# Performance work log

Hardware: AMD Instinct MI355X
Metric: run time of the kernel (lower is better)

Reference implementation:

```python
import jax, jax.numpy as jnp
import numpy as np

INPUT_DIM = 1024
OUTPUT_DIM = 1024
DEGREE = 8


def setup_inputs() -> dict:
    key = jax.random.key(0)
    k1, k2 = jax.random.split(key)
    x = jax.random.normal(k1, (8192, INPUT_DIM), dtype=jnp.float32)
    std = 1.0 / (INPUT_DIM * (DEGREE + 1))
    cheby_coeffs = jax.random.normal(k2, (INPUT_DIM, OUTPUT_DIM, DEGREE + 1), dtype=jnp.float32) * std
    return {"x": x, "cheby_coeffs": cheby_coeffs}


def reference(x, cheby_coeffs):
    # x: [B, I]; cheby_coeffs: [I, O, D+1]
    degree = cheby_coeffs.shape[-1] - 1
    t = jnp.clip(jnp.tanh(x), -0.999, 0.999)            # [B, I]
    theta = jnp.arccos(t)[..., None]                     # [B, I, 1]
    arange = jnp.arange(degree + 1, dtype=x.dtype)       # [D+1]
    basis = jnp.cos(theta * arange)                      # [B, I, D+1] Chebyshev T_d(t)
    y = jnp.einsum('bid,iod->bo', basis, cheby_coeffs)   # [B, O]
    return y
```

## Files before the change

kernel.cpp:

```cpp
#include <hip/hip_runtime.h>
#include <stdint.h>

#define B_ROWS 8192
#define I_DIM  1024
#define N_DIM  1024
#define NDEG   9
#define K_DIM  (I_DIM * (NDEG-1))

#define BM 256
#define BN 128
#define BK 64
#define NT (K_DIM / BK)

typedef __attribute__((ext_vector_type(8)))  short short8;
typedef __attribute__((ext_vector_type(16))) float f32x16;

__device__ __forceinline__ unsigned short f2bf(float f) {
  union { float f; uint32_t u; } v; v.f = f;
  uint32_t u = v.u;
  u += 0x7FFFu + ((u >> 16) & 1u);
  return (unsigned short)(u >> 16);
}

__device__ __forceinline__ float bf2f(unsigned short h) {
  union { uint32_t u; float f; } v; v.u = ((uint32_t)h) << 16;
  return v.f;
}

__device__ __forceinline__ float fast_tanh(float x) {
  float e = __expf(2.0f * x);
  return 1.0f - __fdividef(2.0f, e + 1.0f);
}

__device__ __forceinline__ int h2(int r) { return (r >> 2) & 7; }

__global__ __launch_bounds__(256) void prep_kernel(const float* __restrict__ x,
                                                   const float* __restrict__ cf,
                                                   unsigned short* __restrict__ A,
                                                   unsigned short* __restrict__ Bt,
                                                   float* __restrict__ bias,
                                                   int repack_blocks) {
  __shared__ unsigned short L[32][584];
  const int tid = threadIdx.x;

  if ((int)blockIdx.x < repack_blocks) {
    const int bx = blockIdx.x;
    const int i0 = (bx & 31) * 32;
    const int o0 = (bx >> 5) * 64;

    #pragma unroll
    for (int j = 0; j < 18; ++j) {
      const int f4  = j * 256 + tid;
      const int il  = f4 / 144;
      const int odq = f4 % 144;
      const float4 v = *reinterpret_cast<const float4*>(
          cf + ((size_t)(i0 + il) * N_DIM + o0) * NDEG + (size_t)odq * 4);
      ushort4 w;
      w.x = f2bf(v.x); w.y = f2bf(v.y); w.z = f2bf(v.z); w.w = f2bf(v.w);
      *reinterpret_cast<ushort4*>(&L[il][odq * 4]) = w;
    }
    __syncthreads();

    for (int od = tid; od < 576; od += 256) {
      const int o = od / 9, d = od % 9;
      if (d == 0) {
        float s = 0.f;
        #pragma unroll
        for (int il = 0; il < 32; ++il) s += bf2f(L[il][od]);
        atomicAdd(&bias[o0 + o], s);
      } else {
        const size_t base = (size_t)(o0 + o) * K_DIM + (size_t)(d - 1) * I_DIM + i0;
        #pragma unroll
        for (int ci = 0; ci < 4; ++ci) {
          uint32_t uu[4];
          #pragma unroll
          for (int p = 0; p < 4; ++p) {
            unsigned short lo = L[ci * 8 + p * 2 + 0][od];
            unsigned short hi = L[ci * 8 + p * 2 + 1][od];
            uu[p] = (uint32_t)lo | ((uint32_t)hi << 16);
          }
          uint4 u; u.x = uu[0]; u.y = uu[1]; u.z = uu[2]; u.w = uu[3];
          *reinterpret_cast<uint4*>(Bt + base + ci * 8) = u;
        }
      }
    }
  } else {
    const int b  = ((int)blockIdx.x - repack_blocks) * 2 + (tid >> 7);
    const int j  = tid & 127;
    const int i0 = j * 8;
    const float4 xv0 = *reinterpret_cast<const float4*>(x + (size_t)b * I_DIM + i0);
    const float4 xv1 = *reinterpret_cast<const float4*>(x + (size_t)b * I_DIM + i0 + 4);
    float t[8];
    t[0] = fast_tanh(xv0.x); t[1] = fast_tanh(xv0.y);
    t[2] = fast_tanh(xv0.z); t[3] = fast_tanh(xv0.w);
    t[4] = fast_tanh(xv1.x); t[5] = fast_tanh(xv1.y);
    t[6] = fast_tanh(xv1.z); t[7] = fast_tanh(xv1.w);
    #pragma unroll
    for (int p = 0; p < 8; ++p) t[p] = fminf(fmaxf(t[p], -0.999f), 0.999f);

    unsigned short* outb = A + (size_t)b * K_DIM + i0;
    float Tp[8], Tc[8];
    #pragma unroll
    for (int p = 0; p < 8; ++p) { Tp[p] = 1.f; Tc[p] = t[p]; }
    #pragma unroll
    for (int d = 1; d < NDEG; ++d) {
      short8 o;
      #pragma unroll
      for (int p = 0; p < 8; ++p) o[p] = (short)f2bf(Tc[p]);
      *reinterpret_cast<short8*>(outb + (size_t)(d - 1) * I_DIM) = o;
      if (d < NDEG - 1) {
        #pragma unroll
        for (int p = 0; p < 8; ++p) {
          float Tn = 2.0f * t[p] * Tc[p] - Tp[p];
          Tp[p] = Tc[p]; Tc[p] = Tn;
        }
      }
    }
  }
}

__global__ __launch_bounds__(512, 2) void gemm_kernel(const unsigned short* __restrict__ A,
                                                      const unsigned short* __restrict__ Bt,
                                                      const float* __restrict__ bias,
                                                      float* __restrict__ C) {
  extern __shared__ unsigned short sm[];
  const int tid  = threadIdx.x;
  const int lane = tid & 63;
  const int wave = tid >> 6;
  const int l31  = lane & 31;
  const int half = lane >> 5;
  const int wm   = wave >> 1;
  const int wn   = wave & 1;
  const int m0   = blockIdx.x * BM;
  const int n0   = blockIdx.y * BN;

  const int sr   = tid >> 3;
  const int slot = tid & 7;

  const unsigned short* Abase = A  + (size_t)m0 * K_DIM;
  const unsigned short* Bbase = Bt + (size_t)n0 * K_DIM;

  f32x16 acc[2][2];
  #pragma unroll
  for (int a = 0; a < 2; ++a)
    #pragma unroll
    for (int b = 0; b < 2; ++b)
      #pragma unroll
      for (int r = 0; r < 16; ++r)
        acc[a][b][r] = 0.f;

#define STAGE_A(s, bf, kk) { const int r_ = (s)*64 + sr; const int gc_ = slot ^ h2(r_);     \
    __builtin_amdgcn_global_load_lds(                                                       \
        (const __attribute__((address_space(1))) void*)(Abase + (size_t)r_*K_DIM + (kk) + gc_*8), \
        (__attribute__((address_space(3))) void*)&sm[(bf)*16384 + r_*64 + slot*8], 16, 0, 0); }
#define STAGE_B(s, bf, kk) { const int r_ = (s)*64 + sr; const int gc_ = slot ^ h2(r_);     \
    __builtin_amdgcn_global_load_lds(                                                       \
        (const __attribute__((address_space(1))) void*)(Bbase + (size_t)r_*K_DIM + (kk) + gc_*8), \
        (__attribute__((address_space(3))) void*)&sm[32768 + (bf)*8192 + r_*64 + slot*8], 16, 0, 0); }
#define STAGE6(bf, kk) { STAGE_A(0, bf, kk) STAGE_A(1, bf, kk) STAGE_A(2, bf, kk) STAGE_A(3, bf, kk) \
                         STAGE_B(0, bf, kk) STAGE_B(1, bf, kk) }

  const int rowA0 = wm * 64 + l31;
  const int rowA1 = wm * 64 + 32 + l31;
  const int rowB0 = wn * 64 + l31;
  const int rowB1 = wn * 64 + 32 + l31;
  const int hA0 = h2(rowA0), hA1 = h2(rowA1), hB0 = h2(rowB0), hB1 = h2(rowB1);

  STAGE6(0, 0)
  asm volatile("s_waitcnt vmcnt(0)" ::: "memory");
  __builtin_amdgcn_s_barrier();

  for (int kt = 0; kt < NT; ++kt) {
    const int  cur  = kt & 1;
    const int  nxt  = cur ^ 1;
    const bool more = (kt + 1 < NT);
    const unsigned short* Asc = &sm[cur * 16384];
    const unsigned short* Bsc = &sm[32768 + cur * 8192];

    if (more) { STAGE6(nxt, (kt + 1) * BK) }
    __builtin_amdgcn_sched_barrier(0);

    short8 av[2][4], bv[2][4];
#define READ4(ks) {                                                                          \
    const int c_ = (ks) * 2 + half;                                                          \
    av[0][ks] = *reinterpret_cast<const short8*>(&Asc[rowA0 * 64 + (c_ ^ hA0) * 8]);         \
    av[1][ks] = *reinterpret_cast<const short8*>(&Asc[rowA1 * 64 + (c_ ^ hA1) * 8]);         \
    bv[0][ks] = *reinterpret_cast<const short8*>(&Bsc[rowB0 * 64 + (c_ ^ hB0) * 8]);         \
    bv[1][ks] = *reinterpret_cast<const short8*>(&Bsc[rowB1 * 64 + (c_ ^ hB1) * 8]); }

    READ4(0)
    #pragma unroll
    for (int ks = 0; ks < 4; ++ks) {
      if (ks < 3) READ4(ks + 1)
      acc[0][0] = __builtin_amdgcn_mfma_f32_32x32x16_bf16(av[0][ks], bv[0][ks], acc[0][0], 0, 0, 0);
      acc[0][1] = __builtin_amdgcn_mfma_f32_32x32x16_bf16(av[0][ks], bv[1][ks], acc[0][1], 0, 0, 0);
      acc[1][0] = __builtin_amdgcn_mfma_f32_32x32x16_bf16(av[1][ks], bv[0][ks], acc[1][0], 0, 0, 0);
      acc[1][1] = __builtin_amdgcn_mfma_f32_32x32x16_bf16(av[1][ks], bv[1][ks], acc[1][1], 0, 0, 0);
      if (ks < 3) __builtin_amdgcn_sched_group_barrier(0x100, 4, 0);
      __builtin_amdgcn_sched_group_barrier(0x008, 4, 0);
    }
#undef READ4

    if (more) {
      asm volatile("s_waitcnt vmcnt(0)" ::: "memory");
      __builtin_amdgcn_s_barrier();
    }
  }
#undef STAGE_A
#undef STAGE_B
#undef STAGE6

  #pragma unroll
  for (int ni = 0; ni < 2; ++ni) {
    const int col  = n0 + wn * 64 + ni * 32 + l31;
    const float bc = bias[col];
    #pragma unroll
    for (int mi = 0; mi < 2; ++mi) {
      const int rbase = m0 + wm * 64 + mi * 32 + 4 * half;
      #pragma unroll
      for (int r = 0; r < 16; ++r) {
        const int row = rbase + (r & 3) + 8 * (r >> 2);
        C[(size_t)row * N_DIM + col] = acc[mi][ni][r] + bc;
      }
    }
  }
}

extern "C" void kernel_launch(void* const* d_in, const int* in_sizes, int n_in,
                              void* d_out, int out_size, void* d_ws, size_t ws_size,
                              hipStream_t stream) {
  const float* x      = (const float*)d_in[0];
  const float* coeffs = (const float*)d_in[1];
  float* y            = (float*)d_out;

  const size_t bt_bytes = (size_t)N_DIM * K_DIM * sizeof(unsigned short);
  unsigned short* Bt = (unsigned short*)d_ws;
  float* bias        = (float*)((char*)d_ws + bt_bytes);
  unsigned short* A  = (unsigned short*)((char*)d_ws + bt_bytes + 4096);

  hipMemsetAsync(bias, 0, N_DIM * sizeof(float), stream);

  hipFuncSetAttribute((const void*)gemm_kernel,
                      hipFuncAttributeMaxDynamicSharedMemorySize, 98304);

  size_t avail    = (ws_size > bt_bytes + 4096) ? (ws_size - bt_bytes - 4096) : 0;
  size_t rows_fit = avail / ((size_t)K_DIM * sizeof(unsigned short));
  int m_chunk = (int)((rows_fit / BM) * BM);
  if (m_chunk > B_ROWS) m_chunk = B_ROWS;
  if (m_chunk < BM)     m_chunk = BM;

  for (int m0 = 0; m0 < B_ROWS; m0 += m_chunk) {
    int mc = B_ROWS - m0; if (mc > m_chunk) mc = m_chunk;
    const int rb = (m0 == 0) ? 512 : 0;
    prep_kernel<<<rb + mc / 2, 256, 0, stream>>>(x + (size_t)m0 * I_DIM, coeffs, A, Bt, bias, rb);
    gemm_kernel<<<dim3(mc / BM, N_DIM / BN), 512, 98304, stream>>>(
        A, Bt, bias, y + (size_t)m0 * N_DIM);
  }
}
```

Baseline: 263.9 us.

## Fuse Chebyshev basis generation into GEMM A-tile staging, interleave K by input

The bf16 basis matrix A is no longer materialized in global memory. Each GEMM block loads x directly, computes tanh and the Chebyshev recurrence, and writes packed bf16 tiles into LDS. K is reordered so that each input's 8 degrees are contiguous, with the weight repack changed to match. Block indices are also remapped for L2 locality. This removes the large write and re-read of A, at the cost of redundant basis computation across N tiles and an extra sync per K step.

```diff
diff --git a/kernel.cpp b/kernel.cpp
--- a/kernel.cpp
+++ b/kernel.cpp
@@ -27,6 +27,12 @@
   return v.f;
 }
 
+__device__ __forceinline__ uint32_t pk_bf16(float lo, float hi) {
+  uint32_t r;
+  asm("v_cvt_pk_bf16_f32 %0, %1, %2" : "=v"(r) : "v"(lo), "v"(hi));
+  return r;
+}
+
 __device__ __forceinline__ float fast_tanh(float x) {
   float e = __expf(2.0f * x);
   return 1.0f - __fdividef(2.0f, e + 1.0f);
@@ -34,92 +40,49 @@
 
 __device__ __forceinline__ int h2(int r) { return (r >> 2) & 7; }
 
-__global__ __launch_bounds__(256) void prep_kernel(const float* __restrict__ x,
-                                                   const float* __restrict__ cf,
-                                                   unsigned short* __restrict__ A,
-                                                   unsigned short* __restrict__ Bt,
-                                                   float* __restrict__ bias,
-                                                   int repack_blocks) {
+__global__ __launch_bounds__(256) void repack_kernel(const float* __restrict__ cf,
+                                                     unsigned short* __restrict__ Bt,
+                                                     float* __restrict__ bias) {
   __shared__ unsigned short L[32][584];
+  const int i0  = blockIdx.x * 32;
+  const int o0  = blockIdx.y * 64;
   const int tid = threadIdx.x;
 
-  if ((int)blockIdx.x < repack_blocks) {
-    const int bx = blockIdx.x;
-    const int i0 = (bx & 31) * 32;
-    const int o0 = (bx >> 5) * 64;
-
-    #pragma unroll
-    for (int j = 0; j < 18; ++j) {
-      const int f4  = j * 256 + tid;
-      const int il  = f4 / 144;
-      const int odq = f4 % 144;
-      const float4 v = *reinterpret_cast<const float4*>(
-          cf + ((size_t)(i0 + il) * N_DIM + o0) * NDEG + (size_t)odq * 4);
-      ushort4 w;
-      w.x = f2bf(v.x); w.y = f2bf(v.y); w.z = f2bf(v.z); w.w = f2bf(v.w);
-      *reinterpret_cast<ushort4*>(&L[il][odq * 4]) = w;
-    }
-    __syncthreads();
-
-    for (int od = tid; od < 576; od += 256) {
-      const int o = od / 9, d = od % 9;
-      if (d == 0) {
-        float s = 0.f;
-        #pragma unroll
-        for (int il = 0; il < 32; ++il) s += bf2f(L[il][od]);
-        atomicAdd(&bias[o0 + o], s);
-      } else {
-        const size_t base = (size_t)(o0 + o) * K_DIM + (size_t)(d - 1) * I_DIM + i0;
-        #pragma unroll
-        for (int ci = 0; ci < 4; ++ci) {
-          uint32_t uu[4];
-          #pragma unroll
-          for (int p = 0; p < 4; ++p) {
-            unsigned short lo = L[ci * 8 + p * 2 + 0][od];
-            unsigned short hi = L[ci * 8 + p * 2 + 1][od];
-            uu[p] = (uint32_t)lo | ((uint32_t)hi << 16);
-          }
-          uint4 u; u.x = uu[0]; u.y = uu[1]; u.z = uu[2]; u.w = uu[3];
-          *reinterpret_cast<uint4*>(Bt + base + ci * 8) = u;
-        }
-      }
-    }
-  } else {
-    const int b  = ((int)blockIdx.x - repack_blocks) * 2 + (tid >> 7);
-    const int j  = tid & 127;
-    const int i0 = j * 8;
-    const float4 xv0 = *reinterpret_cast<const float4*>(x + (size_t)b * I_DIM + i0);
-    const float4 xv1 = *reinterpret_cast<const float4*>(x + (size_t)b * I_DIM + i0 + 4);
-    float t[8];
-    t[0] = fast_tanh(xv0.x); t[1] = fast_tanh(xv0.y);
-    t[2] = fast_tanh(xv0.z); t[3] = fast_tanh(xv0.w);
-    t[4] = fast_tanh(xv1.x); t[5] = fast_tanh(xv1.y);
-    t[6] = fast_tanh(xv1.z); t[7] = fast_tanh(xv1.w);
-    #pragma unroll
-    for (int p = 0; p < 8; ++p) t[p] = fminf(fmaxf(t[p], -0.999f), 0.999f);
-
-    unsigned short* outb = A + (size_t)b * K_DIM + i0;
-    float Tp[8], Tc[8];
-    #pragma unroll
-    for (int p = 0; p < 8; ++p) { Tp[p] = 1.f; Tc[p] = t[p]; }
-    #pragma unroll
-    for (int d = 1; d < NDEG; ++d) {
-      short8 o;
-      #pragma unroll
-      for (int p = 0; p < 8; ++p) o[p] = (short)f2bf(Tc[p]);
-      *reinterpret_cast<short8*>(outb + (size_t)(d - 1) * I_DIM) = o;
-      if (d < NDEG - 1) {
-        #pragma unroll
-        for (int p = 0; p < 8; ++p) {
-          float Tn = 2.0f * t[p] * Tc[p] - Tp[p];
-          Tp[p] = Tc[p]; Tc[p] = Tn;
-        }
-      }
-    }
-  }
-}
-
-__global__ __launch_bounds__(512, 2) void gemm_kernel(const unsigned short* __restrict__ A,
+  #pragma unroll
+  for (int j = 0; j < 18; ++j) {
+    const int f4  = j * 256 + tid;
+    const int il  = f4 / 144;
+    const int odq = f4 % 144;
+    const float4 v = *reinterpret_cast<const float4*>(
+        cf + ((size_t)(i0 + il) * N_DIM + o0) * NDEG + (size_t)odq * 4);
+    ushort4 w;
+    w.x = f2bf(v.x); w.y = f2bf(v.y); w.z = f2bf(v.z); w.w = f2bf(v.w);
+    *reinterpret_cast<ushort4*>(&L[il][odq * 4]) = w;
+  }
+  __syncthreads();
+
+  const int o  = tid >> 2;
+  const int ci = tid & 3;
+  const size_t base = (size_t)(o0 + o) * K_DIM + (size_t)(i0 + ci * 8) * 8;
+  #pragma unroll
+  for (int p = 0; p < 8; ++p) {
+    const int il = ci * 8 + p;
+    uint4 u;
+    u.x = (uint32_t)L[il][o*9 + 1] | ((uint32_t)L[il][o*9 + 2] << 16);
+    u.y = (uint32_t)L[il][o*9 + 3] | ((uint32_t)L[il][o*9 + 4] << 16);
+    u.z = (uint32_t)L[il][o*9 + 5] | ((uint32_t)L[il][o*9 + 6] << 16);
+    u.w = (uint32_t)L[il][o*9 + 7] | ((uint32_t)L[il][o*9 + 8] << 16);
+    *reinterpret_cast<uint4*>(Bt + base + (size_t)p * 8) = u;
+  }
+  if (tid < 64) {
+    float s = 0.f;
+    #pragma unroll
+    for (int il = 0; il < 32; ++il) s += bf2f(L[il][tid * 9]);
+    atomicAdd(&bias[o0 + tid], s);
+  }
+}
+
+__global__ __launch_bounds__(512, 2) void gemm_kernel(const float* __restrict__ x,
                                                       const unsigned short* __restrict__ Bt,
                                                       const float* __restrict__ bias,
                                                       float* __restrict__ C) {
@@ -131,13 +94,16 @@
   const int half = lane >> 5;
   const int wm   = wave >> 1;
   const int wn   = wave & 1;
-  const int m0   = blockIdx.x * BM;
-  const int n0   = blockIdx.y * BN;
+
+  const int bid = blockIdx.x;
+  const int mt  = (bid & 7) + 8 * (bid >> 6);
+  const int nt  = (bid >> 3) & 7;
+  const int m0  = mt * BM;
+  const int n0  = nt * BN;
 
   const int sr   = tid >> 3;
   const int slot = tid & 7;
 
-  const unsigned short* Abase = A  + (size_t)m0 * K_DIM;
   const unsigned short* Bbase = Bt + (size_t)n0 * K_DIM;
 
   f32x16 acc[2][2];
@@ -149,26 +115,48 @@
       for (int r = 0; r < 16; ++r)
         acc[a][b][r] = 0.f;
 
-#define STAGE_A(s, bf, kk) { const int r_ = (s)*64 + sr; const int gc_ = slot ^ h2(r_);     \
-    __builtin_amdgcn_global_load_lds(                                                       \
-        (const __attribute__((address_space(1))) void*)(Abase + (size_t)r_*K_DIM + (kk) + gc_*8), \
-        (__attribute__((address_space(3))) void*)&sm[(bf)*16384 + r_*64 + slot*8], 16, 0, 0); }
 #define STAGE_B(s, bf, kk) { const int r_ = (s)*64 + sr; const int gc_ = slot ^ h2(r_);     \
     __builtin_amdgcn_global_load_lds(                                                       \
         (const __attribute__((address_space(1))) void*)(Bbase + (size_t)r_*K_DIM + (kk) + gc_*8), \
         (__attribute__((address_space(3))) void*)&sm[32768 + (bf)*8192 + r_*64 + slot*8], 16, 0, 0); }
-#define STAGE6(bf, kk) { STAGE_A(0, bf, kk) STAGE_A(1, bf, kk) STAGE_A(2, bf, kk) STAGE_A(3, bf, kk) \
-                         STAGE_B(0, bf, kk) STAGE_B(1, bf, kk) }
+
+#define LOADX(xr, tt) {                                                                     \
+    _Pragma("unroll")                                                                       \
+    for (int q = 0; q < 4; ++q)                                                             \
+      xr[q] = x[(size_t)(m0 + q*64 + sr) * I_DIM + (tt)*8 + slot]; }
+
+#define BASIS(bf, xr) {                                                                     \
+    _Pragma("unroll")                                                                       \
+    for (int q = 0; q < 4; ++q) {                                                           \
+      const int r_ = q*64 + sr;                                                             \
+      float t = fast_tanh(xr[q]);                                                           \
+      t = fminf(fmaxf(t, -0.999f), 0.999f);                                                 \
+      const float t2 = t + t;                                                               \
+      const float T1 = t;                                                                   \
+      const float T2 = t2*t - 1.0f;                                                         \
+      const float T3 = t2*T2 - T1;                                                          \
+      const float T4 = t2*T3 - T2;                                                          \
+      const float T5 = t2*T4 - T3;                                                          \
+      const float T6 = t2*T5 - T4;                                                          \
+      const float T7 = t2*T6 - T5;                                                          \
+      const float T8 = t2*T7 - T6;                                                          \
+      uint4 u;                                                                              \
+      u.x = pk_bf16(T1, T2); u.y = pk_bf16(T3, T4);                                         \
+      u.z = pk_bf16(T5, T6); u.w = pk_bf16(T7, T8);                                         \
+      *reinterpret_cast<uint4*>(&sm[(bf)*16384 + r_*64 + ((slot ^ h2(r_)))*8]) = u;         \
+    } }
+
+  { STAGE_B(0, 0, 0) STAGE_B(1, 0, 0) }
+  float xr[4];
+  LOADX(xr, 0)
+  BASIS(0, xr)
+  __syncthreads();
 
   const int rowA0 = wm * 64 + l31;
   const int rowA1 = wm * 64 + 32 + l31;
   const int rowB0 = wn * 64 + l31;
   const int rowB1 = wn * 64 + 32 + l31;
   const int hA0 = h2(rowA0), hA1 = h2(rowA1), hB0 = h2(rowB0), hB1 = h2(rowB1);
-
-  STAGE6(0, 0)
-  asm volatile("s_waitcnt vmcnt(0)" ::: "memory");
-  __builtin_amdgcn_s_barrier();
 
   for (int kt = 0; kt < NT; ++kt) {
     const int  cur  = kt & 1;
@@ -177,7 +165,7 @@
     const unsigned short* Asc = &sm[cur * 16384];
     const unsigned short* Bsc = &sm[32768 + cur * 8192];
 
-    if (more) { STAGE6(nxt, (kt + 1) * BK) }
+    if (more) { STAGE_B(0, nxt, (kt + 1) * BK) STAGE_B(1, nxt, (kt + 1) * BK) LOADX(xr, kt + 1) }
     __builtin_amdgcn_sched_barrier(0);
 
     short8 av[2][4], bv[2][4];
@@ -201,14 +189,14 @@
     }
 #undef READ4
 
-    if (more) {
-      asm volatile("s_waitcnt vmcnt(0)" ::: "memory");
-      __builtin_amdgcn_s_barrier();
-    }
-  }
-#undef STAGE_A
+    __builtin_amdgcn_sched_barrier(0);
+    if (more) BASIS(nxt, xr)
+
+    __syncthreads();
+  }
 #undef STAGE_B
-#undef STAGE6
+#undef LOADX
+#undef BASIS
 
   #pragma unroll
   for (int ni = 0; ni < 2; ++ni) {
@@ -236,24 +224,12 @@
   const size_t bt_bytes = (size_t)N_DIM * K_DIM * sizeof(unsigned short);
   unsigned short* Bt = (unsigned short*)d_ws;
   float* bias        = (float*)((char*)d_ws + bt_bytes);
-  unsigned short* A  = (unsigned short*)((char*)d_ws + bt_bytes + 4096);
 
   hipMemsetAsync(bias, 0, N_DIM * sizeof(float), stream);
 
   hipFuncSetAttribute((const void*)gemm_kernel,
                       hipFuncAttributeMaxDynamicSharedMemorySize, 98304);
 
-  size_t avail    = (ws_size > bt_bytes + 4096) ? (ws_size - bt_bytes - 4096) : 0;
-  size_t rows_fit = avail / ((size_t)K_DIM * sizeof(unsigned short));
-  int m_chunk = (int)((rows_fit / BM) * BM);
-  if (m_chunk > B_ROWS) m_chunk = B_ROWS;
-  if (m_chunk < BM)     m_chunk = BM;
-
-  for (int m0 = 0; m0 < B_ROWS; m0 += m_chunk) {
-    int mc = B_ROWS - m0; if (mc > m_chunk) mc = m_chunk;
-    const int rb = (m0 == 0) ? 512 : 0;
-    prep_kernel<<<rb + mc / 2, 256, 0, stream>>>(x + (size_t)m0 * I_DIM, coeffs, A, Bt, bias, rb);
-    gemm_kernel<<<dim3(mc / BM, N_DIM / BN), 512, 98304, stream>>>(
-        A, Bt, bias, y + (size_t)m0 * N_DIM);
-  }
-}
+  repack_kernel<<<dim3(I_DIM / 32, N_DIM / 64), 256, 0, stream>>>(coeffs, Bt, bias);
+  gemm_kernel<<<(B_ROWS / BM) * (N_DIM / BN), 512, 98304, stream>>>(x, Bt, bias, y);
+}
```

New measurement: 293.7 us. 11.3% more time.
